# Performance work log

Measured on AMD Instinct MI355X. Metric: run time of the kernel, lower is better.

## Reference

```python
import jax, jax.numpy as jnp
import numpy as np

NUM_USERS = 100000
NUM_ITEMS = 50000
N_NODES = NUM_USERS + NUM_ITEMS
LATENT_DIM = 64
N_LAYERS = 3
NNZ = 2400000
BATCH = 16384


def setup_inputs() -> dict:
    key = jax.random.key(0)
    k1, k2, k3, k4, k5, k6, k7 = jax.random.split(key, 7)
    user_emb = jax.random.normal(k1, (NUM_USERS, LATENT_DIM), dtype=jnp.float32) * 0.1
    item_emb = jax.random.normal(k2, (NUM_ITEMS, LATENT_DIM), dtype=jnp.float32) * 0.1
    edge_rows = jax.random.randint(k3, (NNZ,), 0, N_NODES, dtype=jnp.int32)
    edge_cols = jax.random.randint(k4, (NNZ,), 0, N_NODES, dtype=jnp.int32)
    # normalized-adjacency-like positive weights
    edge_vals = jax.random.uniform(k5, (NNZ,), dtype=jnp.float32) * 0.05
    user_input = jax.random.randint(k6, (BATCH,), 0, NUM_USERS, dtype=jnp.int64)
    item_input = jax.random.randint(k7, (BATCH,), 0, NUM_ITEMS, dtype=jnp.int64)
    return {
        "user_emb": user_emb,
        "item_emb": item_emb,
        "edge_rows": edge_rows,
        "edge_cols": edge_cols,
        "edge_vals": edge_vals,
        "user_input": user_input,
        "item_input": item_input,
    }


def _spmm(edge_rows, edge_cols, edge_vals, x):
    # sparse [N,N] @ dense [N,D] via gather + weighted segment-sum
    gathered = x[edge_cols] * edge_vals[:, None]  # [nnz, D]
    return jax.ops.segment_sum(gathered, edge_rows, num_segments=N_NODES)


def reference(user_emb, item_emb, edge_rows, edge_cols, edge_vals, user_input, item_input):
    all_emb = jnp.concatenate([user_emb, item_emb], axis=0)  # [N, D]
    acc = all_emb
    for _ in range(N_LAYERS):
        all_emb = _spmm(edge_rows, edge_cols, edge_vals, all_emb)
        acc = acc + all_emb
    light_out = acc / (N_LAYERS + 1)  # mean over stacked layer embeddings
    users_avg = light_out[:NUM_USERS]
    items_avg = light_out[NUM_USERS:]
    u = users_avg[user_input]  # [B, D]
    i = items_avg[item_input]  # [B, D]
    preds = jnp.sum(u * i, axis=1)  # [B]
    return preds
```

## Files before the change

kernel.cpp:

```cpp
#include <hip/hip_runtime.h>

#define NUM_USERS 100000
#define NUM_ITEMS 50000
#define N_NODES   150000
#define DIM       64
#define BATCH_N   16384
#define NPART     586
#define SC_PASSES 8
#define SC_SLICE  18750

__global__ __launch_bounds__(256) void lg_init(const float4* __restrict__ user_emb,
                        const float4* __restrict__ item_emb,
                        float4* __restrict__ x,
                        float4* __restrict__ acc) {
    const long user4 = (long)NUM_USERS * DIM / 4;
    const long tot4  = (long)N_NODES  * DIM / 4;
    for (long i = blockIdx.x * (long)blockDim.x + threadIdx.x;
         i < tot4;
         i += (long)gridDim.x * blockDim.x) {
        float4 v = (i < user4) ? user_emb[i] : item_emb[i - user4];
        x[i]   = v;
        acc[i] = v;
    }
}

__global__ __launch_bounds__(256) void lg_hist(const int* __restrict__ rows,
                                               int* __restrict__ cnt, int nnz) {
    int e = blockIdx.x * blockDim.x + threadIdx.x;
    if (e < nnz) atomicAdd(&cnt[rows[e]], 1);
}

__global__ __launch_bounds__(256) void lg_scan1(const int* __restrict__ cnt,
                                                int* __restrict__ ptr,
                                                int* __restrict__ part) {
    __shared__ int s[256];
    int i = blockIdx.x * 256 + threadIdx.x;
    int v = (i < N_NODES) ? cnt[i] : 0;
    s[threadIdx.x] = v;
    __syncthreads();
    #pragma unroll
    for (int off = 1; off < 256; off <<= 1) {
        int t = (threadIdx.x >= off) ? s[threadIdx.x - off] : 0;
        __syncthreads();
        s[threadIdx.x] += t;
        __syncthreads();
    }
    if (i < N_NODES) ptr[i] = s[threadIdx.x] - v;
    if (threadIdx.x == 255) part[blockIdx.x] = s[255];
}

__global__ __launch_bounds__(64) void lg_scan2(int* __restrict__ part, int n) {
    int lane = threadIdx.x & 63;
    int run = 0;
    for (int base = 0; base < n; base += 64) {
        int i = base + lane;
        int v = (i < n) ? part[i] : 0;
        int orig = v;
        #pragma unroll
        for (int off = 1; off < 64; off <<= 1) {
            int t = __shfl_up(v, off, 64);
            if (lane >= off) v += t;
        }
        if (i < n) part[i] = run + v - orig;
        run += __shfl(v, 63, 64);
    }
}

__global__ __launch_bounds__(256) void lg_scan3(int* __restrict__ ptr,
                                                const int* __restrict__ part,
                                                int* __restrict__ cur) {
    int i = blockIdx.x * 256 + threadIdx.x;
    if (i < N_NODES) {
        int p = ptr[i] + part[blockIdx.x];
        ptr[i] = p;
        cur[i] = p;
    }
}

__global__ __launch_bounds__(256) void lg_scatter_pass(const int* __restrict__ rows,
                           const int* __restrict__ cols,
                           const float* __restrict__ vals, int* __restrict__ cur,
                           int2* __restrict__ edges, int nnz, int lo, int hi) {
    int e = blockIdx.x * blockDim.x + threadIdx.x;
    if (e >= nnz) return;
    int r = rows[e];
    if (r < lo || r >= hi) return;
    int pos = atomicAdd(&cur[r], 1);
    edges[pos] = make_int2(cols[e], __float_as_int(vals[e]));
}

template <bool WRITE_Y>
__global__ __launch_bounds__(256) void lg_spmm_csr(const int* __restrict__ ptr,
                            const int* __restrict__ cnt,
                            const int2* __restrict__ edges,
                            const float* __restrict__ x, float* __restrict__ y,
                            float* __restrict__ acc) {
    int r    = blockIdx.x * (blockDim.x >> 6) + (threadIdx.x >> 6);
    int lane = threadIdx.x & 63;
    if (r >= N_NODES) return;
    int start = __builtin_amdgcn_readfirstlane(ptr[r]);
    int len   = __builtin_amdgcn_readfirstlane(cnt[r]);
    const int2* __restrict__ ep = edges + start;
    float s0 = 0.0f, s1 = 0.0f, s2 = 0.0f, s3 = 0.0f;
    int j = 0;
    for (; j + 4 <= len; j += 4) {
        int2 e0 = ep[j];
        int2 e1 = ep[j + 1];
        int2 e2 = ep[j + 2];
        int2 e3 = ep[j + 3];
        s0 += __int_as_float(e0.y) * x[(e0.x << 6) + lane];
        s1 += __int_as_float(e1.y) * x[(e1.x << 6) + lane];
        s2 += __int_as_float(e2.y) * x[(e2.x << 6) + lane];
        s3 += __int_as_float(e3.y) * x[(e3.x << 6) + lane];
    }
    for (; j < len; ++j) {
        int2 e0 = ep[j];
        s0 += __int_as_float(e0.y) * x[(e0.x << 6) + lane];
    }
    float sum = (s0 + s1) + (s2 + s3);
    int o = (r << 6) + lane;
    if (WRITE_Y) y[o] = sum;
    acc[o] += sum;
}

__global__ __launch_bounds__(256) void lg_dot(const float* __restrict__ acc,
                       const int*   __restrict__ uidx,
                       const int*   __restrict__ iidx,
                       float*       __restrict__ out,
                       int batch) {
    int b    = blockIdx.x * (blockDim.x >> 6) + (threadIdx.x >> 6);
    int lane = threadIdx.x & 63;
    if (b >= batch) return;
    int u = uidx[b];
    int t = NUM_USERS + iidx[b];
    float p = acc[(u << 6) + lane] * acc[(t << 6) + lane] * (1.0f / 16.0f);
    #pragma unroll
    for (int off = 32; off > 0; off >>= 1)
        p += __shfl_down(p, off, 64);
    if (lane == 0) out[b] = p;
}

extern "C" void kernel_launch(void* const* d_in, const int* in_sizes, int n_in,
                              void* d_out, int out_size, void* d_ws, size_t ws_size,
                              hipStream_t stream) {
    const float* user_emb  = (const float*)d_in[0];
    const float* item_emb  = (const float*)d_in[1];
    const int*   edge_rows = (const int*)  d_in[2];
    const int*   edge_cols = (const int*)  d_in[3];
    const float* edge_vals = (const float*)d_in[4];
    const int*   user_inp  = (const int*)  d_in[5];
    const int*   item_inp  = (const int*)  d_in[6];
    float*       out       = (float*)d_out;

    const int nnz = in_sizes[2];

    const size_t embBytes = (size_t)N_NODES * DIM * sizeof(float);
    const size_t nodeInts = (size_t)N_NODES * sizeof(int);
    const size_t need = 3 * embBytes + (size_t)nnz * 8 + 3 * nodeInts
                      + (size_t)NPART * sizeof(int);
    if (ws_size < need) return;

    char* ws = (char*)d_ws;
    float* x     = (float*)(ws);
    float* y     = (float*)(ws + embBytes);
    float* acc   = (float*)(ws + 2 * embBytes);
    int2*  edges = (int2*) (ws + 3 * embBytes);
    int*   cnt   = (int*)  (ws + 3 * embBytes + (size_t)nnz * 8);
    int*   ptr   = (int*)  (ws + 3 * embBytes + (size_t)nnz * 8 + nodeInts);
    int*   cur   = (int*)  (ws + 3 * embBytes + (size_t)nnz * 8 + 2 * nodeInts);
    int*   part  = (int*)  (ws + 3 * embBytes + (size_t)nnz * 8 + 3 * nodeInts);

    lg_init<<<2048, 256, 0, stream>>>((const float4*)user_emb,
                                      (const float4*)item_emb,
                                      (float4*)x, (float4*)acc);

    hipMemsetAsync(cnt, 0, nodeInts, stream);
    const int eb = (nnz + 255) / 256;
    lg_hist <<<eb,    256, 0, stream>>>(edge_rows, cnt, nnz);
    lg_scan1<<<NPART, 256, 0, stream>>>(cnt, ptr, part);
    lg_scan2<<<1,      64, 0, stream>>>(part, NPART);
    lg_scan3<<<NPART, 256, 0, stream>>>(ptr, part, cur);
    for (int p = 0; p < SC_PASSES; ++p) {
        lg_scatter_pass<<<eb, 256, 0, stream>>>(edge_rows, edge_cols, edge_vals,
                                                cur, edges, nnz,
                                                p * SC_SLICE, (p + 1) * SC_SLICE);
    }

    const int rowBlocks = (N_NODES + 3) / 4;
    lg_spmm_csr<true ><<<rowBlocks, 256, 0, stream>>>(ptr, cnt, edges, x, y, acc);
    lg_spmm_csr<true ><<<rowBlocks, 256, 0, stream>>>(ptr, cnt, edges, y, x, acc);
    lg_spmm_csr<false><<<rowBlocks, 256, 0, stream>>>(ptr, cnt, edges, x, y, acc);

    lg_dot<<<(BATCH_N + 3) / 4, 256, 0, stream>>>(acc, user_inp, item_inp,
                                                  out, BATCH_N);
}
```

Baseline: 666.3 us.

## Bucket edges once before scatter and drop accumulator buffer traffic

```diff
diff --git a/kernel.cpp b/kernel.cpp
--- a/kernel.cpp
+++ b/kernel.cpp
@@ -6,23 +6,8 @@
 #define DIM       64
 #define BATCH_N   16384
 #define NPART     586
-#define SC_PASSES 8
+#define NBUCK     8
 #define SC_SLICE  18750
-
-__global__ __launch_bounds__(256) void lg_init(const float4* __restrict__ user_emb,
-                        const float4* __restrict__ item_emb,
-                        float4* __restrict__ x,
-                        float4* __restrict__ acc) {
-    const long user4 = (long)NUM_USERS * DIM / 4;
-    const long tot4  = (long)N_NODES  * DIM / 4;
-    for (long i = blockIdx.x * (long)blockDim.x + threadIdx.x;
-         i < tot4;
-         i += (long)gridDim.x * blockDim.x) {
-        float4 v = (i < user4) ? user_emb[i] : item_emb[i - user4];
-        x[i]   = v;
-        acc[i] = v;
-    }
-}
 
 __global__ __launch_bounds__(256) void lg_hist(const int* __restrict__ rows,
                                                int* __restrict__ cnt, int nnz) {
@@ -77,25 +62,55 @@
     }
 }
 
-__global__ __launch_bounds__(256) void lg_scatter_pass(const int* __restrict__ rows,
+__global__ void lg_bcur(const int* __restrict__ ptr, int* __restrict__ bcur) {
+    int t = threadIdx.x;
+    if (t < NBUCK) bcur[t] = ptr[t * SC_SLICE];
+}
+
+__global__ __launch_bounds__(256) void lg_bucket(const int* __restrict__ rows,
                            const int* __restrict__ cols,
-                           const float* __restrict__ vals, int* __restrict__ cur,
-                           int2* __restrict__ edges, int nnz, int lo, int hi) {
-    int e = blockIdx.x * blockDim.x + threadIdx.x;
-    if (e >= nnz) return;
-    int r = rows[e];
-    if (r < lo || r >= hi) return;
+                           const float* __restrict__ vals,
+                           int* __restrict__ bcur,
+                           int* __restrict__ brow, int2* __restrict__ bcv, int nnz) {
+    __shared__ int hist[NBUCK], base[NBUCK], off[NBUCK];
+    if (threadIdx.x < NBUCK) { hist[threadIdx.x] = 0; off[threadIdx.x] = 0; }
+    __syncthreads();
+    int e = blockIdx.x * 256 + threadIdx.x;
+    int r = 0, b = -1;
+    if (e < nnz) { r = rows[e]; b = r / SC_SLICE; atomicAdd(&hist[b], 1); }
+    __syncthreads();
+    if (threadIdx.x < NBUCK && hist[threadIdx.x] > 0)
+        base[threadIdx.x] = atomicAdd(&bcur[threadIdx.x], hist[threadIdx.x]);
+    __syncthreads();
+    if (b >= 0) {
+        int rank = atomicAdd(&off[b], 1);
+        int pos  = base[b] + rank;
+        brow[pos] = r;
+        bcv[pos]  = make_int2(cols[e], __float_as_int(vals[e]));
+    }
+}
+
+__global__ __launch_bounds__(256) void lg_scatter2(const int* __restrict__ brow,
+                           const int2* __restrict__ bcv,
+                           const int* __restrict__ ptr, int* __restrict__ cur,
+                           int2* __restrict__ edges, int b, int nnz) {
+    int lo = __builtin_amdgcn_readfirstlane(ptr[b * SC_SLICE]);
+    int hi = (b == NBUCK - 1) ? nnz
+             : __builtin_amdgcn_readfirstlane(ptr[(b + 1) * SC_SLICE]);
+    int i = lo + blockIdx.x * 256 + threadIdx.x;
+    if (i >= hi) return;
+    int r = brow[i];
     int pos = atomicAdd(&cur[r], 1);
-    edges[pos] = make_int2(cols[e], __float_as_int(vals[e]));
-}
-
-template <bool WRITE_Y>
-__global__ __launch_bounds__(256) void lg_spmm_csr(const int* __restrict__ ptr,
+    edges[pos] = bcv[i];
+}
+
+__global__ __launch_bounds__(256) void lg_spmm(const int* __restrict__ ptr,
                             const int* __restrict__ cnt,
                             const int2* __restrict__ edges,
-                            const float* __restrict__ x, float* __restrict__ y,
-                            float* __restrict__ acc) {
-    int r    = blockIdx.x * (blockDim.x >> 6) + (threadIdx.x >> 6);
+                            const float* __restrict__ xu,
+                            const float* __restrict__ xi,
+                            float* __restrict__ yout) {
+    int r    = blockIdx.x * 4 + (threadIdx.x >> 6);
     int lane = threadIdx.x & 63;
     if (r >= N_NODES) return;
     int start = __builtin_amdgcn_readfirstlane(ptr[r]);
@@ -103,41 +118,61 @@
     const int2* __restrict__ ep = edges + start;
     float s0 = 0.0f, s1 = 0.0f, s2 = 0.0f, s3 = 0.0f;
     int j = 0;
-    for (; j + 4 <= len; j += 4) {
-        int2 e0 = ep[j];
-        int2 e1 = ep[j + 1];
-        int2 e2 = ep[j + 2];
-        int2 e3 = ep[j + 3];
-        s0 += __int_as_float(e0.y) * x[(e0.x << 6) + lane];
-        s1 += __int_as_float(e1.y) * x[(e1.x << 6) + lane];
-        s2 += __int_as_float(e2.y) * x[(e2.x << 6) + lane];
-        s3 += __int_as_float(e3.y) * x[(e3.x << 6) + lane];
+    for (; j + 8 <= len; j += 8) {
+        int2 m0 = ep[j];     int2 m1 = ep[j + 1];
+        int2 m2 = ep[j + 2]; int2 m3 = ep[j + 3];
+        int2 m4 = ep[j + 4]; int2 m5 = ep[j + 5];
+        int2 m6 = ep[j + 6]; int2 m7 = ep[j + 7];
+        const float* b0 = (m0.x < NUM_USERS) ? xu : xi;
+        const float* b1 = (m1.x < NUM_USERS) ? xu : xi;
+        const float* b2 = (m2.x < NUM_USERS) ? xu : xi;
+        const float* b3 = (m3.x < NUM_USERS) ? xu : xi;
+        const float* b4 = (m4.x < NUM_USERS) ? xu : xi;
+        const float* b5 = (m5.x < NUM_USERS) ? xu : xi;
+        const float* b6 = (m6.x < NUM_USERS) ? xu : xi;
+        const float* b7 = (m7.x < NUM_USERS) ? xu : xi;
+        s0 += __int_as_float(m0.y) * b0[(m0.x << 6) + lane];
+        s1 += __int_as_float(m1.y) * b1[(m1.x << 6) + lane];
+        s2 += __int_as_float(m2.y) * b2[(m2.x << 6) + lane];
+        s3 += __int_as_float(m3.y) * b3[(m3.x << 6) + lane];
+        s0 += __int_as_float(m4.y) * b4[(m4.x << 6) + lane];
+        s1 += __int_as_float(m5.y) * b5[(m5.x << 6) + lane];
+        s2 += __int_as_float(m6.y) * b6[(m6.x << 6) + lane];
+        s3 += __int_as_float(m7.y) * b7[(m7.x << 6) + lane];
     }
     for (; j < len; ++j) {
-        int2 e0 = ep[j];
-        s0 += __int_as_float(e0.y) * x[(e0.x << 6) + lane];
+        int2 m = ep[j];
+        const float* b = (m.x < NUM_USERS) ? xu : xi;
+        s0 += __int_as_float(m.y) * b[(m.x << 6) + lane];
     }
     float sum = (s0 + s1) + (s2 + s3);
-    int o = (r << 6) + lane;
-    if (WRITE_Y) y[o] = sum;
-    acc[o] += sum;
-}
-
-__global__ __launch_bounds__(256) void lg_dot(const float* __restrict__ acc,
+    yout[(r << 6) + lane] = sum;
+}
+
+__global__ __launch_bounds__(256) void lg_dot4(const float* __restrict__ ue,
+                       const float* __restrict__ ie,
+                       const float* __restrict__ x1,
+                       const float* __restrict__ x2,
+                       const float* __restrict__ x3,
                        const int*   __restrict__ uidx,
                        const int*   __restrict__ iidx,
                        float*       __restrict__ out,
                        int batch) {
-    int b    = blockIdx.x * (blockDim.x >> 6) + (threadIdx.x >> 6);
+    int bb   = blockIdx.x * 4 + (threadIdx.x >> 6);
     int lane = threadIdx.x & 63;
-    if (b >= batch) return;
-    int u = uidx[b];
-    int t = NUM_USERS + iidx[b];
-    float p = acc[(u << 6) + lane] * acc[(t << 6) + lane] * (1.0f / 16.0f);
+    if (bb >= batch) return;
+    int u = uidx[bb];
+    int i = iidx[bb];
+    int t = NUM_USERS + i;
+    int uo = (u << 6) + lane;
+    int to = (t << 6) + lane;
+    float au = ue[(u << 6) + lane] + x1[uo] + x2[uo] + x3[uo];
+    float at = ie[(i << 6) + lane] + x1[to] + x2[to] + x3[to];
+    float p  = au * at * (1.0f / 16.0f);
     #pragma unroll
     for (int off = 32; off > 0; off >>= 1)
         p += __shfl_down(p, off, 64);
-    if (lane == 0) out[b] = p;
+    if (lane == 0) out[bb] = p;
 }
 
 extern "C" void kernel_launch(void* const* d_in, const int* in_sizes, int n_in,
@@ -157,22 +192,21 @@
     const size_t embBytes = (size_t)N_NODES * DIM * sizeof(float);
     const size_t nodeInts = (size_t)N_NODES * sizeof(int);
     const size_t need = 3 * embBytes + (size_t)nnz * 8 + 3 * nodeInts
-                      + (size_t)NPART * sizeof(int);
+                      + (size_t)(NPART + NBUCK) * sizeof(int);
     if (ws_size < need) return;
 
     char* ws = (char*)d_ws;
-    float* x     = (float*)(ws);
-    float* y     = (float*)(ws + embBytes);
-    float* acc   = (float*)(ws + 2 * embBytes);
+    float* x1    = (float*)(ws);
+    float* x2    = (float*)(ws + embBytes);
+    float* x3    = (float*)(ws + 2 * embBytes);
     int2*  edges = (int2*) (ws + 3 * embBytes);
     int*   cnt   = (int*)  (ws + 3 * embBytes + (size_t)nnz * 8);
     int*   ptr   = (int*)  (ws + 3 * embBytes + (size_t)nnz * 8 + nodeInts);
     int*   cur   = (int*)  (ws + 3 * embBytes + (size_t)nnz * 8 + 2 * nodeInts);
     int*   part  = (int*)  (ws + 3 * embBytes + (size_t)nnz * 8 + 3 * nodeInts);
-
-    lg_init<<<2048, 256, 0, stream>>>((const float4*)user_emb,
-                                      (const float4*)item_emb,
-                                      (float4*)x, (float4*)acc);
+    int*   bcur  = part + NPART;
+    int*   brow  = (int*)x1;
+    int2*  bcv   = (int2*)((char*)x1 + (size_t)nnz * 4);
 
     hipMemsetAsync(cnt, 0, nodeInts, stream);
     const int eb = (nnz + 255) / 256;
@@ -180,17 +214,19 @@
     lg_scan1<<<NPART, 256, 0, stream>>>(cnt, ptr, part);
     lg_scan2<<<1,      64, 0, stream>>>(part, NPART);
     lg_scan3<<<NPART, 256, 0, stream>>>(ptr, part, cur);
-    for (int p = 0; p < SC_PASSES; ++p) {
-        lg_scatter_pass<<<eb, 256, 0, stream>>>(edge_rows, edge_cols, edge_vals,
-                                                cur, edges, nnz,
-                                                p * SC_SLICE, (p + 1) * SC_SLICE);
-    }
+    lg_bcur <<<1,      64, 0, stream>>>(ptr, bcur);
+    lg_bucket<<<eb,   256, 0, stream>>>(edge_rows, edge_cols, edge_vals,
+                                        bcur, brow, bcv, nnz);
+    const int sgrid = (nnz / NBUCK + nnz / 64 + 255) / 256;
+    for (int b = 0; b < NBUCK; ++b)
+        lg_scatter2<<<sgrid, 256, 0, stream>>>(brow, bcv, ptr, cur, edges, b, nnz);
 
     const int rowBlocks = (N_NODES + 3) / 4;
-    lg_spmm_csr<true ><<<rowBlocks, 256, 0, stream>>>(ptr, cnt, edges, x, y, acc);
-    lg_spmm_csr<true ><<<rowBlocks, 256, 0, stream>>>(ptr, cnt, edges, y, x, acc);
-    lg_spmm_csr<false><<<rowBlocks, 256, 0, stream>>>(ptr, cnt, edges, x, y, acc);
-
-    lg_dot<<<(BATCH_N + 3) / 4, 256, 0, stream>>>(acc, user_inp, item_inp,
-                                                  out, BATCH_N);
-}
+    const float* xi_shift = item_emb - (size_t)NUM_USERS * DIM;
+    lg_spmm<<<rowBlocks, 256, 0, stream>>>(ptr, cnt, edges, user_emb, xi_shift, x1);
+    lg_spmm<<<rowBlocks, 256, 0, stream>>>(ptr, cnt, edges, x1, x1, x2);
+    lg_spmm<<<rowBlocks, 256, 0, stream>>>(ptr, cnt, edges, x2, x2, x3);
+
+    lg_dot4<<<(BATCH_N + 3) / 4, 256, 0, stream>>>(user_emb, item_emb, x1, x2, x3,
+                                                   user_inp, item_inp, out, BATCH_N);
+}
```

After: 740.7 us. +11.2%, slower.
